# Kernel tuning notes

Measured on AMD Instinct MI355X. Metric: run time of the kernel, lower is better.

Reference implementation:

```python
import jax, jax.numpy as jnp
import numpy as np

D_MODEL = 1024
N_HEAD = 16
HEAD_DIM = D_MODEL // N_HEAD


def setup_inputs() -> dict:
    key = jax.random.key(0)
    ks = jax.random.split(key, 5)
    B, T = 2, 2048
    s = 1.0 / np.sqrt(D_MODEL)
    return {
        "x": jax.random.normal(ks[0], (B, T, D_MODEL), dtype=jnp.float32),
        "w_qkv": jax.random.normal(ks[1], (D_MODEL, 3 * D_MODEL), dtype=jnp.float32) * s,
        "b_qkv": jnp.zeros((3 * D_MODEL,), dtype=jnp.float32),
        "w_proj": jax.random.normal(ks[2], (D_MODEL, D_MODEL), dtype=jnp.float32) * s,
        "b_proj": jnp.zeros((D_MODEL,), dtype=jnp.float32),
    }


def reference(x, w_qkv, b_qkv, w_proj, b_proj):
    B, T, C = x.shape
    H, Dh = N_HEAD, HEAD_DIM
    scale = Dh ** -0.5
    qkv = x @ w_qkv + b_qkv                      # [B,T,3C]
    q, k, v = jnp.split(qkv, 3, axis=2)
    # [B,T,C] -> [B,H,T,Dh]
    q = q.reshape(B, T, H, Dh).transpose(0, 2, 1, 3)
    k = k.reshape(B, T, H, Dh).transpose(0, 2, 1, 3)
    v = v.reshape(B, T, H, Dh).transpose(0, 2, 1, 3)
    att = jnp.einsum("bhqd,bhkd->bhqk", q, k) * scale  # [B,H,T,T]
    causal = jnp.tril(jnp.ones((T, T), dtype=bool))
    att = jnp.where(causal, att, -jnp.inf)
    att = jax.nn.softmax(att, axis=-1)
    out = jnp.einsum("bhqk,bhkd->bhqd", att, v)  # [B,H,T,Dh]
    out = out.transpose(0, 2, 1, 3).reshape(B, T, C)
    return out @ w_proj + b_proj
```

## Files before the change

kernel.cpp:

```cpp
#include <hip/hip_runtime.h>
#include <hip/hip_bf16.h>

#define B_ 2
#define T_ 2048
#define C_ 1024
#define H_ 16
#define DH_ 64

typedef __attribute__((ext_vector_type(8))) short bf16x8;
typedef __attribute__((ext_vector_type(4))) float f32x4;
typedef __attribute__((ext_vector_type(4))) unsigned int u32x4;

#define DEVI static __device__ __forceinline__

DEVI unsigned short f2bf(float f) {
  unsigned int u = __float_as_uint(f);
  u = (u + 0x7fffu + ((u >> 16) & 1u)) >> 16;
  return (unsigned short)u;
}

DEVI f32x4 mfma16(bf16x8 a, bf16x8 b, f32x4 c) {
  return __builtin_amdgcn_mfma_f32_16x16x32_bf16(a, b, c, 0, 0, 0);
}

DEVI void gload_lds16(const unsigned short* g, unsigned short* l) {
  __builtin_amdgcn_global_load_lds(
      (const __attribute__((address_space(1))) unsigned int*)g,
      (__attribute__((address_space(3))) unsigned int*)l, 16, 0, 0);
}

DEVI unsigned int cvtpk_bf16(float lo, float hi) {
  unsigned int r;
  asm("v_cvt_pk_bf16_f32 %0, %1, %2" : "=v"(r) : "v"(lo), "v"(hi));
  return r;
}

DEVI int kperm(int kv) {
  return (kv & 3) | (((kv >> 3) & 1) << 2) | (((kv >> 5) & 1) << 3) |
         (((kv >> 2) & 1) << 4) | (((kv >> 4) & 1) << 5);
}

__global__ __launch_bounds__(256) void prep_kernel(
    const float* __restrict__ x, const float* __restrict__ w_qkv,
    const float* __restrict__ w_proj, unsigned short* __restrict__ xb,
    unsigned short* __restrict__ wqkvT, unsigned short* __restrict__ wprojT) {
  __shared__ float tile[32][33];
  int b = blockIdx.x, tid = threadIdx.x;
  if (b < 4096) {
    int i = b * 256 + tid;
    float4 v = reinterpret_cast<const float4*>(x)[i];
    ushort4 o;
    o.x = f2bf(v.x); o.y = f2bf(v.y); o.z = f2bf(v.z); o.w = f2bf(v.w);
    reinterpret_cast<ushort4*>(xb)[i] = o;
  } else {
    const float* in;
    unsigned short* out;
    int R, C, bb;
    if (b < 7168) { bb = b - 4096; in = w_qkv; out = wqkvT; R = 1024; C = 3072; }
    else          { bb = b - 7168; in = w_proj; out = wprojT; R = 1024; C = 1024; }
    int nbx = C >> 5;
    int c0 = (bb % nbx) * 32, r0 = (bb / nbx) * 32;
    int tx = tid & 31, ty = tid >> 5;
#pragma unroll
    for (int j = 0; j < 32; j += 8)
      tile[ty + j][tx] = in[(size_t)(r0 + ty + j) * C + c0 + tx];
    __syncthreads();
#pragma unroll
    for (int j = 0; j < 32; j += 8)
      out[(size_t)(c0 + ty + j) * R + r0 + tx] = f2bf(tile[tx][ty + j]);
  }
}

__global__ __launch_bounds__(512, 2) void gemm256_qkv(
    const unsigned short* __restrict__ A, const unsigned short* __restrict__ Bt,
    const float* __restrict__ bias,
    unsigned short* __restrict__ qbuf, unsigned short* __restrict__ kbuf,
    unsigned short* __restrict__ vtbuf) {
  __shared__ __attribute__((aligned(16))) unsigned short As[2][256 * 64];
  __shared__ __attribute__((aligned(16))) unsigned short Bs[2][256 * 64];
  const int Kd = 1024;
  int tid = threadIdx.x;
  int lane = tid & 63, w = tid >> 6;
  int wm = w >> 2, wn = w & 3;
  int lrow = lane & 15, lgrp = lane >> 4;

  int g = blockIdx.x;
  int gs = (g & 7) * 24 + (g >> 3);
  int by = gs / 12, bx = gs % 12;
  int bm = by * 256, bn = bx * 256;
  const unsigned short* Ab = A + (size_t)bm * Kd;
  const unsigned short* Bb = Bt + (size_t)bn * Kd;

  int sL[2], scl[2];
#pragma unroll
  for (int it = 0; it < 2; ++it) {
    int c = tid + it * 512;
    int L = c >> 3, s = c & 7, v = s ^ (L & 7);
    sL[it] = L;
    scl[it] = (v >> 2) * 32 + (v & 3) * 8;
  }

  auto stgA = [&](int t, int h) {
    unsigned short* dst = As[t & 1] + h * 8192;
    int k0 = t << 6;
#pragma unroll
    for (int it = 0; it < 2; ++it)
      gload_lds16(Ab + (size_t)(h * 128 + sL[it]) * Kd + k0 + scl[it],
                  dst + (tid + it * 512) * 8);
  };
  auto stgB = [&](int t, int h) {
    unsigned short* dst = Bs[t & 1] + h * 8192;
    int k0 = t << 6;
#pragma unroll
    for (int it = 0; it < 2; ++it)
      gload_lds16(Bb + (size_t)(h * 128 + sL[it]) * Kd + k0 + scl[it],
                  dst + (tid + it * 512) * 8);
  };

  auto lda = [&](const unsigned short* buf, int mi, int kk) -> bf16x8 {
    int row = wm * 128 + mi * 16 + lrow;
    int s = ((kk << 2) | lgrp) ^ (row & 7);
    return *reinterpret_cast<const bf16x8*>((const char*)buf + row * 128 + s * 16);
  };
  auto ldb = [&](const unsigned short* buf, int ni, int kk) -> bf16x8 {
    int row = wn * 64 + ni * 16 + lrow;
    int s = ((kk << 2) | lgrp) ^ (row & 7);
    return *reinterpret_cast<const bf16x8*>((const char*)buf + row * 128 + s * 16);
  };

  f32x4 acc[8][4] = {};
  bf16x8 bfr[4][2], af[2][2];

#define PHASE_TAIL                                          \
  __builtin_amdgcn_s_barrier();                             \
  asm volatile("s_waitcnt lgkmcnt(0)" ::: "memory");        \
  __builtin_amdgcn_sched_barrier(0);                        \
  __builtin_amdgcn_s_setprio(1);

#define MFMA_PAIR(base)                                     \
  _Pragma("unroll") for (int ii = 0; ii < 2; ++ii)          \
  _Pragma("unroll") for (int ni = 0; ni < 4; ++ni) {        \
    acc[(base) + ii][ni] = mfma16(af[ii][0], bfr[ni][0], acc[(base) + ii][ni]); \
    acc[(base) + ii][ni] = mfma16(af[ii][1], bfr[ni][1], acc[(base) + ii][ni]); \
  }

#define PHASE_END                                           \
  __builtin_amdgcn_s_setprio(0);                            \
  __builtin_amdgcn_s_barrier();

  stgA(0, 0); stgA(0, 1); stgB(0, 0); stgB(0, 1); stgB(1, 0); stgB(1, 1);
  asm volatile("s_waitcnt vmcnt(4)" ::: "memory");
  __builtin_amdgcn_s_barrier();

#pragma unroll 1
  for (int j = 0; j < 8; ++j) {
    const bool nl = (j < 7);
    const int t1 = 2 * j + 1, t2 = 2 * j + 2, t3 = 2 * j + 3;

#pragma unroll
    for (int ni = 0; ni < 4; ++ni) { bfr[ni][0] = ldb(Bs[0], ni, 0); bfr[ni][1] = ldb(Bs[0], ni, 1); }
    af[0][0] = lda(As[0], 0, 0); af[0][1] = lda(As[0], 0, 1);
    af[1][0] = lda(As[0], 1, 0); af[1][1] = lda(As[0], 1, 1);
    stgA(t1, 0);
    PHASE_TAIL; MFMA_PAIR(0); PHASE_END;

    af[0][0] = lda(As[0], 2, 0); af[0][1] = lda(As[0], 2, 1);
    af[1][0] = lda(As[0], 3, 0); af[1][1] = lda(As[0], 3, 1);
    stgA(t1, 1);
    if (nl) stgB(t2, 0);
    PHASE_TAIL; MFMA_PAIR(2); PHASE_END;

    af[0][0] = lda(As[0], 4, 0); af[0][1] = lda(As[0], 4, 1);
    af[1][0] = lda(As[0], 5, 0); af[1][1] = lda(As[0], 5, 1);
    if (nl) stgB(t2, 1);
    PHASE_TAIL; MFMA_PAIR(4); PHASE_END;

    af[0][0] = lda(As[0], 6, 0); af[0][1] = lda(As[0], 6, 1);
    af[1][0] = lda(As[0], 7, 0); af[1][1] = lda(As[0], 7, 1);
    PHASE_TAIL; MFMA_PAIR(6);
    __builtin_amdgcn_s_setprio(0);
    if (nl) { asm volatile("s_waitcnt vmcnt(4)" ::: "memory"); }
    else    { asm volatile("s_waitcnt vmcnt(0)" ::: "memory"); }
    __builtin_amdgcn_s_barrier();

#pragma unroll
    for (int ni = 0; ni < 4; ++ni) { bfr[ni][0] = ldb(Bs[1], ni, 0); bfr[ni][1] = ldb(Bs[1], ni, 1); }
    af[0][0] = lda(As[1], 0, 0); af[0][1] = lda(As[1], 0, 1);
    af[1][0] = lda(As[1], 1, 0); af[1][1] = lda(As[1], 1, 1);
    if (nl) stgA(t2, 0);
    PHASE_TAIL; MFMA_PAIR(0); PHASE_END;

    af[0][0] = lda(As[1], 2, 0); af[0][1] = lda(As[1], 2, 1);
    af[1][0] = lda(As[1], 3, 0); af[1][1] = lda(As[1], 3, 1);
    if (nl) stgA(t2, 1);
    PHASE_TAIL; MFMA_PAIR(2); PHASE_END;

    af[0][0] = lda(As[1], 4, 0); af[0][1] = lda(As[1], 4, 1);
    af[1][0] = lda(As[1], 5, 0); af[1][1] = lda(As[1], 5, 1);
    if (nl) stgB(t3, 0);
    PHASE_TAIL; MFMA_PAIR(4); PHASE_END;

    af[0][0] = lda(As[1], 6, 0); af[0][1] = lda(As[1], 6, 1);
    af[1][0] = lda(As[1], 7, 0); af[1][1] = lda(As[1], 7, 1);
    if (nl) stgB(t3, 1);
    PHASE_TAIL; MFMA_PAIR(6);
    __builtin_amdgcn_s_setprio(0);
    if (nl) { asm volatile("s_waitcnt vmcnt(4)" ::: "memory"); }
    __builtin_amdgcn_s_barrier();
  }
#undef PHASE_TAIL
#undef MFMA_PAIR
#undef PHASE_END

  int r0 = bm + wm * 128, c0 = bn + wn * 64;
#pragma unroll
  for (int ni = 0; ni < 4; ++ni) {
    int col = c0 + ni * 16 + lrow;
    float bv = bias[col];
    int which = col >> 10, cc = col & 1023;
    int h = cc >> 6, d = cc & 63;
#pragma unroll
    for (int mi = 0; mi < 8; ++mi) {
      int rowb = r0 + mi * 16 + lgrp * 4;
      int b = rowb >> 11, tt = rowb & 2047;
      if (which == 2) {
        ushort4 pk;
        pk.x = f2bf(acc[mi][ni][0] + bv);
        pk.y = f2bf(acc[mi][ni][1] + bv);
        pk.z = f2bf(acc[mi][ni][2] + bv);
        pk.w = f2bf(acc[mi][ni][3] + bv);
        *reinterpret_cast<ushort4*>(vtbuf + ((size_t)((b * 16 + h) * 64 + d)) * T_ + tt) = pk;
      } else {
        unsigned short* dst = (which == 0) ? qbuf : kbuf;
        size_t base = ((size_t)(b * 16 + h) * T_ + tt) * DH_ + d;
#pragma unroll
        for (int r = 0; r < 4; ++r)
          dst[base + (size_t)r * DH_] = f2bf(acc[mi][ni][r] + bv);
      }
    }
  }
}

__global__ __launch_bounds__(256) void gemm_proj(
    const unsigned short* __restrict__ A, const unsigned short* __restrict__ Bt,
    const float* __restrict__ bias, float* __restrict__ outp,
    int Ndim, int Kdim) {
  __shared__ __attribute__((aligned(16))) unsigned short As[128 * 32];
  __shared__ __attribute__((aligned(16))) unsigned short Bs[128 * 32];
  int tid = threadIdx.x;
  int lane = tid & 63, w = tid >> 6;
  int wm = w >> 1, wn = w & 1;
  int lrow = lane & 15, lgrp = lane >> 4;
  int bm = blockIdx.y * 128, bn = blockIdx.x * 128;
  const unsigned short* Ab = A + (size_t)bm * Kdim;
  const unsigned short* Bb = Bt + (size_t)bn * Kdim;

  f32x4 acc[4][4] = {};
  int nk = Kdim >> 5;
  for (int kt = 0; kt < nk; ++kt) {
    int k0 = kt << 5;
    __syncthreads();
#pragma unroll
    for (int it = 0; it < 2; ++it) {
      int c = tid + it * 256;
      int row = c >> 2, kc = (c & 3) << 3;
      gload_lds16(Ab + (size_t)row * Kdim + k0 + kc, As + (size_t)c * 8);
      gload_lds16(Bb + (size_t)row * Kdim + k0 + kc, Bs + (size_t)c * 8);
    }
    __syncthreads();
    bf16x8 af[4], bfr[4];
#pragma unroll
    for (int mi = 0; mi < 4; ++mi)
      af[mi] = *reinterpret_cast<const bf16x8*>(As + (size_t)(wm * 64 + mi * 16 + lrow) * 32 + lgrp * 8);
#pragma unroll
    for (int ni = 0; ni < 4; ++ni)
      bfr[ni] = *reinterpret_cast<const bf16x8*>(Bs + (size_t)(wn * 64 + ni * 16 + lrow) * 32 + lgrp * 8);
#pragma unroll
    for (int mi = 0; mi < 4; ++mi)
#pragma unroll
      for (int ni = 0; ni < 4; ++ni)
        acc[mi][ni] = mfma16(af[mi], bfr[ni], acc[mi][ni]);
  }

  int r0 = bm + wm * 64, c0 = bn + wn * 64;
#pragma unroll
  for (int ni = 0; ni < 4; ++ni) {
    int col = c0 + ni * 16 + lrow;
    float bv = bias[col];
#pragma unroll
    for (int mi = 0; mi < 4; ++mi) {
      int rowb = r0 + mi * 16 + lgrp * 4;
#pragma unroll
      for (int r = 0; r < 4; ++r)
        outp[(size_t)(rowb + r) * Ndim + col] = acc[mi][ni][r] + bv;
    }
  }
}

__global__ __launch_bounds__(256, 4) void attn_kernel(
    const unsigned short* __restrict__ qbuf,
    const unsigned short* __restrict__ kbuf,
    const unsigned short* __restrict__ vtbuf,
    unsigned short* __restrict__ attno) {
  __shared__ __attribute__((aligned(16))) unsigned short Ks[64 * 64];
  __shared__ __attribute__((aligned(16))) unsigned short Vts[64 * 64];

  int tid = threadIdx.x;
  int lane = tid & 63, w = tid >> 6;
  int lrow = lane & 15, lgrp = lane >> 4;

  int g = blockIdx.x;
  int s = g >> 8;
  int p = (g >> 3) & 7;
  int bh = (g & 7) | (((g >> 6) & 3) << 3);
  int qb = (s == 0) ? p : (s == 1) ? (31 - p) : (s == 2) ? (8 + p) : (23 - p);
  int wq0 = qb * 64 + w * 16;
  int nkb = qb + 1;

  const unsigned short* Qb = qbuf + (size_t)bh * T_ * DH_;
  const unsigned short* Kb = kbuf + (size_t)bh * T_ * DH_;
  const unsigned short* Vb = vtbuf + (size_t)bh * DH_ * T_;

  int srow0 = tid >> 3, scol = tid & 7;
  int srow1 = srow0 + 32;
  int pk0 = kperm(srow0), pk1 = kperm(srow1);
  int soffK0 = pk0 * 128 + ((scol * 16) ^ ((pk0 & 7) << 4));
  int soffK1 = pk1 * 128 + ((scol * 16) ^ ((pk1 & 7) << 4));
  int soffV0 = srow0 * 128 + ((scol * 16) ^ ((srow0 & 7) << 4));
  int soffV1 = srow1 * 128 + ((scol * 16) ^ ((srow1 & 7) << 4));

  const float SC = 0.125f * 1.44269504f;
  int kvbase = ((lgrp & 1) << 3) | ((lgrp >> 1) << 5);
  const int koff[4] = {0, 4, 16, 20};

  bf16x8 qf[2];
#pragma unroll
  for (int ks = 0; ks < 2; ++ks)
    qf[ks] = *reinterpret_cast<const bf16x8*>(
        Qb + (size_t)(wq0 + lrow) * DH_ + ks * 32 + lgrp * 8);

  f32x4 o[4] = {};
  float l_run = 0.f;

  bf16x8 sk0, sk1, sv0, sv1;
  auto stage_load = [&](int kb) {
    sk0 = *reinterpret_cast<const bf16x8*>(Kb + (size_t)(kb * 64 + srow0) * DH_ + scol * 8);
    sk1 = *reinterpret_cast<const bf16x8*>(Kb + (size_t)(kb * 64 + srow1) * DH_ + scol * 8);
    sv0 = *reinterpret_cast<const bf16x8*>(Vb + (size_t)srow0 * T_ + kb * 64 + scol * 8);
    sv1 = *reinterpret_cast<const bf16x8*>(Vb + (size_t)srow1 * T_ + kb * 64 + scol * 8);
  };
  auto stage_write = [&]() {
    *reinterpret_cast<bf16x8*>((char*)Ks + soffK0) = sk0;
    *reinterpret_cast<bf16x8*>((char*)Ks + soffK1) = sk1;
    *reinterpret_cast<bf16x8*>((char*)Vts + soffV0) = sv0;
    *reinterpret_cast<bf16x8*>((char*)Vts + soffV1) = sv1;
  };

  stage_load(0);
#pragma unroll 1
  for (int kb = 0; kb < nkb; ++kb) {
    if (kb > 0) __syncthreads();
    stage_write();
    __syncthreads();
    if (kb + 1 < nkb) stage_load(kb + 1);

    f32x4 sreg[4] = {};
#pragma unroll
    for (int ks = 0; ks < 2; ++ks) {
      bf16x8 kf[4];
#pragma unroll
      for (int ni = 0; ni < 4; ++ni) {
        int kr = ni * 16 + lrow;
        int off = kr * 128 + (((ks * 32 + lgrp * 8) * 2) ^ ((kr & 7) << 4));
        kf[ni] = *reinterpret_cast<const bf16x8*>((const char*)Ks + off);
      }
      __builtin_amdgcn_s_setprio(1);
#pragma unroll
      for (int ni = 0; ni < 4; ++ni)
        sreg[ni] = mfma16(kf[ni], qf[ks], sreg[ni]);
      __builtin_amdgcn_s_setprio(0);
    }

    if (kb == qb) {
      int q = wq0 + lrow;
#pragma unroll
      for (int ni = 0; ni < 4; ++ni) {
        int kvb = kb * 64 + kvbase + koff[ni];
#pragma unroll
        for (int r = 0; r < 4; ++r)
          if (kvb + r > q) sreg[ni][r] = -1e30f;
      }
    }

    f32x4 e[4];
#pragma unroll
    for (int ni = 0; ni < 4; ++ni)
#pragma unroll
      for (int r = 0; r < 4; ++r)
        e[ni][r] = __builtin_amdgcn_exp2f(sreg[ni][r] * SC);

    f32x4 ts = (e[0] + e[1]) + (e[2] + e[3]);
    l_run += (ts[0] + ts[1]) + (ts[2] + ts[3]);

    unsigned int Aw[4], Bw[4];
    Aw[0] = cvtpk_bf16(e[0][0], e[0][1]); Aw[1] = cvtpk_bf16(e[0][2], e[0][3]);
    Aw[2] = cvtpk_bf16(e[1][0], e[1][1]); Aw[3] = cvtpk_bf16(e[1][2], e[1][3]);
    Bw[0] = cvtpk_bf16(e[2][0], e[2][1]); Bw[1] = cvtpk_bf16(e[2][2], e[2][3]);
    Bw[2] = cvtpk_bf16(e[3][0], e[3][1]); Bw[3] = cvtpk_bf16(e[3][2], e[3][3]);
    u32x4 p0v, p1v;
#pragma unroll
    for (int ww = 0; ww < 4; ++ww) {
      auto sw = __builtin_amdgcn_permlane32_swap(Aw[ww], Bw[ww], false, false);
      p0v[ww] = sw[0];
      p1v[ww] = sw[1];
    }
    bf16x8 pa[2];
    pa[0] = __builtin_bit_cast(bf16x8, p0v);
    pa[1] = __builtin_bit_cast(bf16x8, p1v);

#pragma unroll
    for (int ks = 0; ks < 2; ++ks) {
      bf16x8 vf[4];
#pragma unroll
      for (int di = 0; di < 4; ++di) {
        int vr = di * 16 + lrow;
        int off = vr * 128 + (((ks * 32 + lgrp * 8) * 2) ^ ((vr & 7) << 4));
        vf[di] = *reinterpret_cast<const bf16x8*>((const char*)Vts + off);
      }
      __builtin_amdgcn_s_setprio(1);
#pragma unroll
      for (int di = 0; di < 4; ++di)
        o[di] = mfma16(pa[ks], vf[di], o[di]);
      __builtin_amdgcn_s_setprio(0);
    }
  }

  float rs = l_run;
  rs += __shfl_xor(rs, 16);
  rs += __shfl_xor(rs, 32);
  float linv = 1.0f / rs;

  int b = bh >> 4, h = bh & 15;
  float lr[4];
#pragma unroll
  for (int r = 0; r < 4; ++r) lr[r] = __shfl(linv, lgrp * 4 + r);
#pragma unroll
  for (int r = 0; r < 4; ++r) {
    int q = wq0 + lgrp * 4 + r;
    size_t base = ((size_t)(b * T_ + q)) * C_ + h * 64 + lrow;
#pragma unroll
    for (int di = 0; di < 4; ++di)
      attno[base + (size_t)di * 16] = f2bf(o[di][r] * lr[r]);
  }
}

extern "C" void kernel_launch(void* const* d_in, const int* in_sizes, int n_in,
                              void* d_out, int out_size, void* d_ws, size_t ws_size,
                              hipStream_t stream) {
  const float* x      = (const float*)d_in[0];
  const float* w_qkv  = (const float*)d_in[1];
  const float* b_qkv  = (const float*)d_in[2];
  const float* w_proj = (const float*)d_in[3];
  const float* b_proj = (const float*)d_in[4];

  char* ws = (char*)d_ws;
  unsigned short* xb     = (unsigned short*)(ws + 0);
  unsigned short* wqkvT  = (unsigned short*)(ws + 8388608);
  unsigned short* wprojT = (unsigned short*)(ws + 14680064);
  unsigned short* qbuf   = (unsigned short*)(ws + 16777216);
  unsigned short* kbuf   = (unsigned short*)(ws + 25165824);
  unsigned short* vtbuf  = (unsigned short*)(ws + 33554432);
  unsigned short* attno  = (unsigned short*)(ws + 41943040);

  prep_kernel<<<8192, 256, 0, stream>>>(x, w_qkv, w_proj, xb, wqkvT, wprojT);
  gemm256_qkv<<<dim3(192), 512, 0, stream>>>(xb, wqkvT, b_qkv, qbuf, kbuf, vtbuf);
  attn_kernel<<<dim3(1024), 256, 0, stream>>>(qbuf, kbuf, vtbuf, attno);
  gemm_proj<<<dim3(8, 32), 256, 0, stream>>>(attno, wprojT, b_proj, (float*)d_out,
                                             1024, 1024);
}
```

Before: 102.1 us.

## Retile QKV GEMM to 128x192 tiles with 4 waves and 512 blocks

Replaces the 256x256 QKV GEMM tile (8 waves, 192 blocks) with a 128x192 tile using 4 waves, each computing 128x48, launched as 512 blocks. The aim is to fill all 256 CUs instead of leaving many idle with only 192 blocks, reducing wave quantization. B staging is split into three 64-row chunks, and the prefetch schedule and vmcnt waits are adjusted to match. In exchange, each tile reuses its loads less, so global and LDS traffic per FLOP goes up.

```diff
diff --git a/kernel.cpp b/kernel.cpp
--- a/kernel.cpp
+++ b/kernel.cpp
@@ -71,65 +71,65 @@
   }
 }
 
-__global__ __launch_bounds__(512, 2) void gemm256_qkv(
+__global__ __launch_bounds__(256, 2) void gemm192_qkv(
     const unsigned short* __restrict__ A, const unsigned short* __restrict__ Bt,
     const float* __restrict__ bias,
     unsigned short* __restrict__ qbuf, unsigned short* __restrict__ kbuf,
     unsigned short* __restrict__ vtbuf) {
-  __shared__ __attribute__((aligned(16))) unsigned short As[2][256 * 64];
-  __shared__ __attribute__((aligned(16))) unsigned short Bs[2][256 * 64];
+  __shared__ __attribute__((aligned(16))) unsigned short As[2][128 * 64];
+  __shared__ __attribute__((aligned(16))) unsigned short Bs[2][192 * 64];
   const int Kd = 1024;
   int tid = threadIdx.x;
   int lane = tid & 63, w = tid >> 6;
-  int wm = w >> 2, wn = w & 3;
+  int wn = w;
   int lrow = lane & 15, lgrp = lane >> 4;
 
   int g = blockIdx.x;
-  int gs = (g & 7) * 24 + (g >> 3);
-  int by = gs / 12, bx = gs % 12;
-  int bm = by * 256, bn = bx * 256;
+  int gs = (g & 7) * 64 + (g >> 3);
+  int by = gs >> 4, bx = gs & 15;
+  int bm = by * 128, bn = bx * 192;
   const unsigned short* Ab = A + (size_t)bm * Kd;
   const unsigned short* Bb = Bt + (size_t)bn * Kd;
 
   int sL[2], scl[2];
 #pragma unroll
   for (int it = 0; it < 2; ++it) {
-    int c = tid + it * 512;
+    int c = tid + it * 256;
     int L = c >> 3, s = c & 7, v = s ^ (L & 7);
     sL[it] = L;
     scl[it] = (v >> 2) * 32 + (v & 3) * 8;
   }
 
   auto stgA = [&](int t, int h) {
-    unsigned short* dst = As[t & 1] + h * 8192;
+    unsigned short* dst = As[t & 1] + h * 4096;
     int k0 = t << 6;
 #pragma unroll
     for (int it = 0; it < 2; ++it)
-      gload_lds16(Ab + (size_t)(h * 128 + sL[it]) * Kd + k0 + scl[it],
-                  dst + (tid + it * 512) * 8);
-  };
-  auto stgB = [&](int t, int h) {
-    unsigned short* dst = Bs[t & 1] + h * 8192;
+      gload_lds16(Ab + (size_t)(h * 64 + sL[it]) * Kd + k0 + scl[it],
+                  dst + (tid + it * 256) * 8);
+  };
+  auto stgB3 = [&](int t, int th) {
+    unsigned short* dst = Bs[t & 1] + th * 4096;
     int k0 = t << 6;
 #pragma unroll
     for (int it = 0; it < 2; ++it)
-      gload_lds16(Bb + (size_t)(h * 128 + sL[it]) * Kd + k0 + scl[it],
-                  dst + (tid + it * 512) * 8);
+      gload_lds16(Bb + (size_t)(th * 64 + sL[it]) * Kd + k0 + scl[it],
+                  dst + (tid + it * 256) * 8);
   };
 
   auto lda = [&](const unsigned short* buf, int mi, int kk) -> bf16x8 {
-    int row = wm * 128 + mi * 16 + lrow;
+    int row = mi * 16 + lrow;
     int s = ((kk << 2) | lgrp) ^ (row & 7);
     return *reinterpret_cast<const bf16x8*>((const char*)buf + row * 128 + s * 16);
   };
   auto ldb = [&](const unsigned short* buf, int ni, int kk) -> bf16x8 {
-    int row = wn * 64 + ni * 16 + lrow;
+    int row = wn * 48 + ni * 16 + lrow;
     int s = ((kk << 2) | lgrp) ^ (row & 7);
     return *reinterpret_cast<const bf16x8*>((const char*)buf + row * 128 + s * 16);
   };
 
-  f32x4 acc[8][4] = {};
-  bf16x8 bfr[4][2], af[2][2];
+  f32x4 acc[8][3] = {};
+  bf16x8 bfr[3][2], af[2][2];
 
 #define PHASE_TAIL                                          \
   __builtin_amdgcn_s_barrier();                             \
@@ -137,9 +137,9 @@
   __builtin_amdgcn_sched_barrier(0);                        \
   __builtin_amdgcn_s_setprio(1);
 
-#define MFMA_PAIR(base)                                     \
+#define MFMA_TRI(base)                                      \
   _Pragma("unroll") for (int ii = 0; ii < 2; ++ii)          \
-  _Pragma("unroll") for (int ni = 0; ni < 4; ++ni) {        \
+  _Pragma("unroll") for (int ni = 0; ni < 3; ++ni) {        \
     acc[(base) + ii][ni] = mfma16(af[ii][0], bfr[ni][0], acc[(base) + ii][ni]); \
     acc[(base) + ii][ni] = mfma16(af[ii][1], bfr[ni][1], acc[(base) + ii][ni]); \
   }
@@ -148,8 +148,10 @@
   __builtin_amdgcn_s_setprio(0);                            \
   __builtin_amdgcn_s_barrier();
 
-  stgA(0, 0); stgA(0, 1); stgB(0, 0); stgB(0, 1); stgB(1, 0); stgB(1, 1);
-  asm volatile("s_waitcnt vmcnt(4)" ::: "memory");
+  stgA(0, 0); stgA(0, 1);
+  stgB3(0, 0); stgB3(0, 1); stgB3(0, 2);
+  stgB3(1, 0); stgB3(1, 1); stgB3(1, 2);
+  asm volatile("s_waitcnt vmcnt(6)" ::: "memory");
   __builtin_amdgcn_s_barrier();
 
 #pragma unroll 1
@@ -158,70 +160,71 @@
     const int t1 = 2 * j + 1, t2 = 2 * j + 2, t3 = 2 * j + 3;
 
 #pragma unroll
-    for (int ni = 0; ni < 4; ++ni) { bfr[ni][0] = ldb(Bs[0], ni, 0); bfr[ni][1] = ldb(Bs[0], ni, 1); }
+    for (int ni = 0; ni < 3; ++ni) { bfr[ni][0] = ldb(Bs[0], ni, 0); bfr[ni][1] = ldb(Bs[0], ni, 1); }
     af[0][0] = lda(As[0], 0, 0); af[0][1] = lda(As[0], 0, 1);
     af[1][0] = lda(As[0], 1, 0); af[1][1] = lda(As[0], 1, 1);
     stgA(t1, 0);
-    PHASE_TAIL; MFMA_PAIR(0); PHASE_END;
+    PHASE_TAIL; MFMA_TRI(0); PHASE_END;
 
     af[0][0] = lda(As[0], 2, 0); af[0][1] = lda(As[0], 2, 1);
     af[1][0] = lda(As[0], 3, 0); af[1][1] = lda(As[0], 3, 1);
     stgA(t1, 1);
-    if (nl) stgB(t2, 0);
-    PHASE_TAIL; MFMA_PAIR(2); PHASE_END;
+    if (nl) stgB3(t2, 0);
+    PHASE_TAIL; MFMA_TRI(2); PHASE_END;
 
     af[0][0] = lda(As[0], 4, 0); af[0][1] = lda(As[0], 4, 1);
     af[1][0] = lda(As[0], 5, 0); af[1][1] = lda(As[0], 5, 1);
-    if (nl) stgB(t2, 1);
-    PHASE_TAIL; MFMA_PAIR(4); PHASE_END;
+    if (nl) stgB3(t2, 1);
+    PHASE_TAIL; MFMA_TRI(4); PHASE_END;
 
     af[0][0] = lda(As[0], 6, 0); af[0][1] = lda(As[0], 6, 1);
     af[1][0] = lda(As[0], 7, 0); af[1][1] = lda(As[0], 7, 1);
-    PHASE_TAIL; MFMA_PAIR(6);
+    if (nl) stgB3(t2, 2);
+    PHASE_TAIL; MFMA_TRI(6);
     __builtin_amdgcn_s_setprio(0);
-    if (nl) { asm volatile("s_waitcnt vmcnt(4)" ::: "memory"); }
+    if (nl) { asm volatile("s_waitcnt vmcnt(6)" ::: "memory"); }
     else    { asm volatile("s_waitcnt vmcnt(0)" ::: "memory"); }
     __builtin_amdgcn_s_barrier();
 
 #pragma unroll
-    for (int ni = 0; ni < 4; ++ni) { bfr[ni][0] = ldb(Bs[1], ni, 0); bfr[ni][1] = ldb(Bs[1], ni, 1); }
+    for (int ni = 0; ni < 3; ++ni) { bfr[ni][0] = ldb(Bs[1], ni, 0); bfr[ni][1] = ldb(Bs[1], ni, 1); }
     af[0][0] = lda(As[1], 0, 0); af[0][1] = lda(As[1], 0, 1);
     af[1][0] = lda(As[1], 1, 0); af[1][1] = lda(As[1], 1, 1);
     if (nl) stgA(t2, 0);
-    PHASE_TAIL; MFMA_PAIR(0); PHASE_END;
+    PHASE_TAIL; MFMA_TRI(0); PHASE_END;
 
     af[0][0] = lda(As[1], 2, 0); af[0][1] = lda(As[1], 2, 1);
     af[1][0] = lda(As[1], 3, 0); af[1][1] = lda(As[1], 3, 1);
-    if (nl) stgA(t2, 1);
-    PHASE_TAIL; MFMA_PAIR(2); PHASE_END;
+    if (nl) { stgA(t2, 1); stgB3(t3, 0); }
+    PHASE_TAIL; MFMA_TRI(2); PHASE_END;
 
     af[0][0] = lda(As[1], 4, 0); af[0][1] = lda(As[1], 4, 1);
     af[1][0] = lda(As[1], 5, 0); af[1][1] = lda(As[1], 5, 1);
-    if (nl) stgB(t3, 0);
-    PHASE_TAIL; MFMA_PAIR(4); PHASE_END;
+    if (nl) stgB3(t3, 1);
+    PHASE_TAIL; MFMA_TRI(4); PHASE_END;
 
     af[0][0] = lda(As[1], 6, 0); af[0][1] = lda(As[1], 6, 1);
     af[1][0] = lda(As[1], 7, 0); af[1][1] = lda(As[1], 7, 1);
-    if (nl) stgB(t3, 1);
-    PHASE_TAIL; MFMA_PAIR(6);
+    if (nl) stgB3(t3, 2);
+    PHASE_TAIL; MFMA_TRI(6);
     __builtin_amdgcn_s_setprio(0);
-    if (nl) { asm volatile("s_waitcnt vmcnt(4)" ::: "memory"); }
+    if (nl) { asm volatile("s_waitcnt vmcnt(6)" ::: "memory"); }
     __builtin_amdgcn_s_barrier();
   }
 #undef PHASE_TAIL
-#undef MFMA_PAIR
+#undef MFMA_TRI
 #undef PHASE_END
 
-  int r0 = bm + wm * 128, c0 = bn + wn * 64;
-#pragma unroll
-  for (int ni = 0; ni < 4; ++ni) {
+  int c0 = bn + wn * 48;
+#pragma unroll
+  for (int ni = 0; ni < 3; ++ni) {
     int col = c0 + ni * 16 + lrow;
     float bv = bias[col];
     int which = col >> 10, cc = col & 1023;
     int h = cc >> 6, d = cc & 63;
 #pragma unroll
     for (int mi = 0; mi < 8; ++mi) {
-      int rowb = r0 + mi * 16 + lgrp * 4;
+      int rowb = bm + mi * 16 + lgrp * 4;
       int b = rowb >> 11, tt = rowb & 2047;
       if (which == 2) {
         ushort4 pk;
@@ -473,7 +476,7 @@
   unsigned short* attno  = (unsigned short*)(ws + 41943040);
 
   prep_kernel<<<8192, 256, 0, stream>>>(x, w_qkv, w_proj, xb, wqkvT, wprojT);
-  gemm256_qkv<<<dim3(192), 512, 0, stream>>>(xb, wqkvT, b_qkv, qbuf, kbuf, vtbuf);
+  gemm192_qkv<<<dim3(512), 256, 0, stream>>>(xb, wqkvT, b_qkv, qbuf, kbuf, vtbuf);
   attn_kernel<<<dim3(1024), 256, 0, stream>>>(qbuf, kbuf, vtbuf, attno);
   gemm_proj<<<dim3(8, 32), 256, 0, stream>>>(attno, wprojT, b_proj, (float*)d_out,
                                              1024, 1024);
```

Result: faster. 98.20 us (-3.8%).
